# Performance work log

Measured on AMD Instinct MI355X. Metric: run time of the kernel, lower is better.

## Reference

```python
import jax, jax.numpy as jnp
import numpy as np

B, T, C, H = 4, 4096, 1024, 64


def setup_inputs() -> dict:
    key = jax.random.key(0)
    k1, k2, k3, k4 = jax.random.split(key, 4)
    x = jax.random.normal(k1, (B, T, C), dtype=jnp.float32)
    # nn.Linear(C, H, bias=False) weights, stored as [C, H] so y = x @ W
    Wq = jax.random.normal(k2, (C, H), dtype=jnp.float32) * (C ** -0.5)
    Wk = jax.random.normal(k3, (C, H), dtype=jnp.float32) * (C ** -0.5)
    Wv = jax.random.normal(k4, (C, H), dtype=jnp.float32) * (C ** -0.5)
    return {"x": x, "Wq": Wq, "Wk": Wk, "Wv": Wv}


def reference(x, Wq, Wk, Wv):
    # x: (B,T,C) -> q,k,v: (B,T,H)
    q = jnp.einsum('btc,ch->bth', x, Wq)
    k = jnp.einsum('btc,ch->bth', x, Wk)
    v = jnp.einsum('btc,ch->bth', x, Wv)
    scale = q.shape[-1] ** -0.5
    # (B,T,T) attention scores with causal mask
    scores = jnp.einsum('bqh,bkh->bqk', q, k) * scale
    t = x.shape[1]
    causal = jnp.tril(jnp.ones((t, t), dtype=bool))
    scores = jnp.where(causal, scores, -jnp.inf)
    attn = jax.nn.softmax(scores, axis=-1)
    return jnp.einsum('bqk,bkh->bqh', attn, v)
```

## Files before the change

kernel.cpp:

```cpp
#include <hip/hip_runtime.h>

#define BATCH 4
#define SEQ   4096
#define CDIM  1024
#define HDIM  64

typedef __attribute__((ext_vector_type(8))) short bf16x8;
typedef __attribute__((ext_vector_type(4))) float f32x4;

#define WT_OFF 0
#define Q_OFF  (3 * HDIM * CDIM)
#define KF_OFF (Q_OFF + BATCH * SEQ * HDIM)
#define VF_OFF (KF_OFF + BATCH * SEQ * HDIM)

static __device__ __forceinline__ short f2bf(float f) {
  union { float f; unsigned u; } a; a.f = f;
  unsigned r = a.u + 0x7fffu + ((a.u >> 16) & 1u);
  return (short)(r >> 16);
}

static __device__ __forceinline__ bf16x8 ld8(const short* p) {
  return *(const bf16x8*)p;
}

__global__ void wcvt_kernel(const float* __restrict__ wq, const float* __restrict__ wk,
                            const float* __restrict__ wv, short* __restrict__ wt2) {
  int idx = blockIdx.x * 256 + threadIdx.x;
  int m = idx >> 16;
  int f = idx & 65535;
  int k0g = f >> 11, hc = (f >> 9) & 3, lr = (f >> 5) & 15, lg = (f >> 3) & 3, j = f & 7;
  int c = k0g * 32 + lg * 8 + j, h = hc * 16 + lr;
  const float* w = (m == 0) ? wq : (m == 1) ? wk : wv;
  wt2[((k0g * 12 + m * 4 + hc) * 64 + lr * 4 + lg) * 8 + j] = f2bf(w[c * 64 + h]);
}

__global__ __launch_bounds__(512, 4) void proj_kernel(const float* __restrict__ x,
                                                      const short* __restrict__ wt2,
                                                      short* __restrict__ ws) {
  __shared__ short xs2[2][32 * 256];
  __shared__ short k_lds[8][16][24];
  __shared__ short v_lds[8][16][24];

  int tid = threadIdx.x;
  int widx = tid >> 6, lane = tid & 63;
  int lr = lane & 15, lg = lane >> 4;
  int row0 = blockIdx.x * 32;
  int rbh = widx >> 2;
  int hcw = widx & 3;

  int sr = tid >> 4, sci = tid & 15;
  const float* xsrc = x + (size_t)(row0 + sr) * CDIM + sci * 4;
  int sxor = (sr & 7) << 4;
  int sbase = sr * 512;

  int rowa = rbh * 16 + lr;
  int abase = rowa * 512;
  int axor = (rowa & 7) << 4;

  const short* bptr = wt2 + (hcw * 64 + lr * 4 + lg) * 8;

  f32x4 acc[3] = {};

#define PLOAD(RG, P) do {                                                    \
    _Pragma("unroll")                                                        \
    for (int q = 0; q < 4; ++q)                                              \
      RG[q] = *(const float4*)(xsrc + (P) * 256 + q * 64);                   \
  } while (0)

#define PSTORE(RG, BUF) do {                                                 \
    char* bc_ = (char*)&xs2[(BUF)][0];                                       \
    _Pragma("unroll")                                                        \
    for (int q = 0; q < 4; ++q) {                                            \
      uint2 u_;                                                              \
      u_.x = (unsigned)(unsigned short)f2bf(RG[q].x) |                       \
             ((unsigned)(unsigned short)f2bf(RG[q].y) << 16);                \
      u_.y = (unsigned)(unsigned short)f2bf(RG[q].z) |                       \
             ((unsigned)(unsigned short)f2bf(RG[q].w) << 16);                \
      *(uint2*)(bc_ + sbase + ((sci * 8 + q * 128) ^ sxor)) = u_;            \
    }                                                                        \
  } while (0)

#define PCOMPUTE(BUF, P) do {                                                \
    const char* bufc_ = (const char*)&xs2[(BUF)][0];                         \
    _Pragma("unroll")                                                        \
    for (int kk = 0; kk < 8; ++kk) {                                         \
      bf16x8 af_ = *(const bf16x8*)(bufc_ + abase + ((kk * 64 + lg * 16) ^ axor)); \
      const short* bk_ = bptr + ((P) * 8 + kk) * 6144;                       \
      _Pragma("unroll")                                                      \
      for (int m = 0; m < 3; ++m) {                                          \
        bf16x8 bf_ = ld8(bk_ + m * 2048);                                    \
        acc[m] = __builtin_amdgcn_mfma_f32_16x16x32_bf16(af_, bf_, acc[m], 0, 0, 0); \
      }                                                                      \
    }                                                                        \
  } while (0)

  {
    float4 rg[4];
    PLOAD(rg, 0);
    PSTORE(rg, 0);
  }
  __syncthreads();
#pragma unroll
  for (int p = 0; p < 4; ++p) {
    float4 rg[4];
    if (p < 3) PLOAD(rg, p + 1);
    PCOMPUTE(p & 1, p);
    if (p < 3) {
      PSTORE(rg, (p + 1) & 1);
      __syncthreads();
    }
  }

  short* qs  = ws + Q_OFF;
  short* kfr = ws + KF_OFF;
  short* vfr = ws + VF_OFF;
  int rbase = row0 + rbh * 16;
#pragma unroll
  for (int reg = 0; reg < 4; ++reg) {
    int t = rbase + lg * 4 + reg;
    qs[t * 64 + hcw * 16 + lr] = f2bf(acc[0][reg]);
    k_lds[widx][lg * 4 + reg][lr] = f2bf(acc[1][reg]);
    v_lds[widx][lr][lg * 4 + reg] = f2bf(acc[2][reg]);
  }
  int b = rbase >> 12;
  int tb = rbase & (SEQ - 1);
  int kb64 = tb >> 6, st = (tb >> 4) & 3;
  if (lane < 32) {
    int i0 = lane >> 1, f8 = (lane & 1) * 8;
    size_t kblk = ((((size_t)b * 64 + kb64) * 4 + st) * 2 + (hcw >> 1)) * 512;
    bf16x8 kv8 = *(const bf16x8*)(&k_lds[widx][i0][f8]);
    *(bf16x8*)(kfr + kblk + ((hcw & 1) * 2 + (f8 >> 3)) * 128 + i0 * 8) = kv8;
    size_t vblk = ((((size_t)b * 64 + kb64) * 2 + ((tb >> 5) & 1)) * 4 + hcw) * 512;
    bf16x8 vv8 = *(const bf16x8*)(&v_lds[widx][i0][f8]);
    *(bf16x8*)(vfr + vblk + (((tb & 16) + f8) >> 3) * 128 + i0 * 8) = vv8;
  }
}

__global__ __launch_bounds__(512, 4) void attn_kernel(const short* __restrict__ ws,
                                                      float* __restrict__ out) {
  __shared__ float p_o[8][4][4][64];
  __shared__ float p_l[8][4][64];
  __shared__ short plds[8][16][72];

  int widx = threadIdx.x >> 6, lane = threadIdx.x & 63;
  int lr = lane & 15, lg = lane >> 4;
  int g = blockIdx.x;

  const short* qs  = ws + Q_OFF;
  const short* kfr = ws + KF_OFF;
  const short* vfr = ws + VF_OFF;
  short* myp = &plds[widx][0][0];

  for (int tt = 0; tt < 2; ++tt) {
    int j = tt == 0 ? g : 1023 - g;
    int t16 = 255 - (j >> 2), b = j & 3;
    int qrow0 = b * SEQ + t16 * 16;
    int nkv = (t16 >> 2) + 1;

    bf16x8 qf0 = ld8(qs + (qrow0 + lr) * 64 + lg * 8);
    bf16x8 qf1 = ld8(qs + (qrow0 + lr) * 64 + 32 + lg * 8);
    const short* kb_b = kfr + (size_t)b * 64 * 4096 + lane * 8;
    const short* vb_b = vfr + (size_t)b * 64 * 4096 + lane * 8;

    f32x4 o[4] = {};
    float l_run[4] = {};

    if (tt) __syncthreads();

    bf16x8 kf[8];
    int kvb = widx;
    if (kvb < nkv) {
      const short* kb = kb_b + (size_t)kvb * 4096;
#pragma unroll
      for (int q8 = 0; q8 < 8; ++q8) kf[q8] = ld8(kb + q8 * 512);
    }

    for (; kvb < nkv; kvb += 8) {
      int kv0 = kvb * 64;

      f32x4 s[4] = {};
#pragma unroll
      for (int st = 0; st < 4; ++st) {
        s[st] = __builtin_amdgcn_mfma_f32_16x16x32_bf16(qf0, kf[st * 2],     s[st], 0, 0, 0);
        s[st] = __builtin_amdgcn_mfma_f32_16x16x32_bf16(qf1, kf[st * 2 + 1], s[st], 0, 0, 0);
      }

      bf16x8 vv[8];
      {
        const short* vb = vb_b + (size_t)kvb * 4096;
#pragma unroll
        for (int q8 = 0; q8 < 8; ++q8) vv[q8] = ld8(vb + q8 * 512);
      }
      int kvn = kvb + 8;
      if (kvn < nkv) {
        const short* kb = kb_b + (size_t)kvn * 4096;
#pragma unroll
        for (int q8 = 0; q8 < 8; ++q8) kf[q8] = ld8(kb + q8 * 512);
      }

      bool last = (kvb == nkv - 1);
#pragma unroll
      for (int reg = 0; reg < 4; ++reg) {
        int ig = t16 * 16 + lg * 4 + reg;
#pragma unroll
        for (int st = 0; st < 4; ++st) {
          float v = s[st][reg] * 0.125f;
          if (last && (kv0 + st * 16 + lr > ig)) v = -1e30f;
          float p = __expf(v);
          l_run[reg] += p;
          myp[(lg * 4 + reg) * 72 + st * 16 + lr] = f2bf(p);
        }
      }
      asm volatile("s_waitcnt lgkmcnt(0)" ::: "memory");
      bf16x8 pf0 = ld8(myp + lr * 72 + lg * 8);
      bf16x8 pf1 = ld8(myp + lr * 72 + 32 + lg * 8);

#pragma unroll
      for (int hc = 0; hc < 4; ++hc) {
        o[hc] = __builtin_amdgcn_mfma_f32_16x16x32_bf16(pf0, vv[hc],     o[hc], 0, 0, 0);
        o[hc] = __builtin_amdgcn_mfma_f32_16x16x32_bf16(pf1, vv[4 + hc], o[hc], 0, 0, 0);
      }
    }

#pragma unroll
    for (int reg = 0; reg < 4; ++reg) {
      float l = l_run[reg];
      l += __shfl_xor(l, 1);
      l += __shfl_xor(l, 2);
      l += __shfl_xor(l, 4);
      l += __shfl_xor(l, 8);
      l_run[reg] = l;
    }

#pragma unroll
    for (int hc = 0; hc < 4; ++hc)
#pragma unroll
      for (int reg = 0; reg < 4; ++reg)
        p_o[widx][hc][reg][lane] = o[hc][reg];
#pragma unroll
    for (int reg = 0; reg < 4; ++reg)
      p_l[widx][reg][lane] = l_run[reg];
    __syncthreads();

    if (widx < 4) {
      int reg = widx;
      float lsum = 0.f;
#pragma unroll
      for (int w = 0; w < 8; ++w) lsum += p_l[w][reg][lane];
      float inv = 1.0f / lsum;
#pragma unroll
      for (int hc = 0; hc < 4; ++hc) {
        float sv = 0.f;
#pragma unroll
        for (int w = 0; w < 8; ++w) sv += p_o[w][hc][reg][lane];
        out[(qrow0 + lg * 4 + reg) * 64 + hc * 16 + lr] = sv * inv;
      }
    }
  }
}

extern "C" void kernel_launch(void* const* d_in, const int* in_sizes, int n_in,
                              void* d_out, int out_size, void* d_ws, size_t ws_size,
                              hipStream_t stream) {
  const float* x  = (const float*)d_in[0];
  const float* wq = (const float*)d_in[1];
  const float* wk = (const float*)d_in[2];
  const float* wv = (const float*)d_in[3];
  short* ws = (short*)d_ws;
  float* out = (float*)d_out;

  wcvt_kernel<<<dim3(768), dim3(256), 0, stream>>>(wq, wk, wv, ws + WT_OFF);
  proj_kernel<<<dim3(512), dim3(512), 0, stream>>>(x, ws + WT_OFF, ws);
  attn_kernel<<<dim3(512), dim3(512), 0, stream>>>(ws, out);
}
```

Before: 67.30 us.

## Split QKV projection across 12 waves, one output tile each, with contiguous x loads

The projection kernel moves from 8 waves to 12 waves per block. Each wave now owns one (matrix, head-chunk) pair and computes both 16-row tiles, so the weight fragment is loaded once per wave and reused across two MFMAs. Before, each wave loaded three weight fragments per A fragment. The x staging loads change from strided float4s to four contiguous float4s per thread, with only the first 512 threads staging. The trade-off is more threads per block, idle staging threads, and higher register and launch-bounds pressure.

```diff
diff --git a/kernel.cpp b/kernel.cpp
--- a/kernel.cpp
+++ b/kernel.cpp
@@ -34,37 +34,36 @@
   wt2[((k0g * 12 + m * 4 + hc) * 64 + lr * 4 + lg) * 8 + j] = f2bf(w[c * 64 + h]);
 }
 
-__global__ __launch_bounds__(512, 4) void proj_kernel(const float* __restrict__ x,
+__global__ __launch_bounds__(768, 6) void proj_kernel(const float* __restrict__ x,
                                                       const short* __restrict__ wt2,
                                                       short* __restrict__ ws) {
   __shared__ short xs2[2][32 * 256];
-  __shared__ short k_lds[8][16][24];
-  __shared__ short v_lds[8][16][24];
+  __shared__ short k_lds[4][2][16][16];
+  __shared__ short v_lds[4][2][16][16];
 
   int tid = threadIdx.x;
   int widx = tid >> 6, lane = tid & 63;
   int lr = lane & 15, lg = lane >> 4;
   int row0 = blockIdx.x * 32;
-  int rbh = widx >> 2;
-  int hcw = widx & 3;
+  int p = widx;
+  int m = p >> 2, hcw = p & 3;
 
   int sr = tid >> 4, sci = tid & 15;
-  const float* xsrc = x + (size_t)(row0 + sr) * CDIM + sci * 4;
+  const float* xsrc = x + (size_t)(row0 + sr) * CDIM + sci * 16;
+  int sbase = sr * 512;
   int sxor = (sr & 7) << 4;
-  int sbase = sr * 512;
-
-  int rowa = rbh * 16 + lr;
-  int abase = rowa * 512;
-  int axor = (rowa & 7) << 4;
-
-  const short* bptr = wt2 + (hcw * 64 + lr * 4 + lg) * 8;
-
-  f32x4 acc[3] = {};
+
+  int abase0 = lr * 512, abase1 = (16 + lr) * 512;
+  int axor = (lr & 7) << 4;
+
+  const short* bptr = wt2 + p * 512 + (lr * 4 + lg) * 8;
+
+  f32x4 acc[2] = {};
 
 #define PLOAD(RG, P) do {                                                    \
     _Pragma("unroll")                                                        \
     for (int q = 0; q < 4; ++q)                                              \
-      RG[q] = *(const float4*)(xsrc + (P) * 256 + q * 64);                   \
+      RG[q] = *(const float4*)(xsrc + (P) * 256 + q * 4);                    \
   } while (0)
 
 #define PSTORE(RG, BUF) do {                                                 \
@@ -76,7 +75,7 @@
              ((unsigned)(unsigned short)f2bf(RG[q].y) << 16);                \
       u_.y = (unsigned)(unsigned short)f2bf(RG[q].z) |                       \
              ((unsigned)(unsigned short)f2bf(RG[q].w) << 16);                \
-      *(uint2*)(bc_ + sbase + ((sci * 8 + q * 128) ^ sxor)) = u_;            \
+      *(uint2*)(bc_ + sbase + ((sci * 32 + q * 8) ^ sxor)) = u_;             \
     }                                                                        \
   } while (0)
 
@@ -84,29 +83,28 @@
     const char* bufc_ = (const char*)&xs2[(BUF)][0];                         \
     _Pragma("unroll")                                                        \
     for (int kk = 0; kk < 8; ++kk) {                                         \
-      bf16x8 af_ = *(const bf16x8*)(bufc_ + abase + ((kk * 64 + lg * 16) ^ axor)); \
-      const short* bk_ = bptr + ((P) * 8 + kk) * 6144;                       \
-      _Pragma("unroll")                                                      \
-      for (int m = 0; m < 3; ++m) {                                          \
-        bf16x8 bf_ = ld8(bk_ + m * 2048);                                    \
-        acc[m] = __builtin_amdgcn_mfma_f32_16x16x32_bf16(af_, bf_, acc[m], 0, 0, 0); \
-      }                                                                      \
+      int co_ = (kk * 64 + lg * 16) ^ axor;                                  \
+      bf16x8 af0_ = *(const bf16x8*)(bufc_ + abase0 + co_);                  \
+      bf16x8 af1_ = *(const bf16x8*)(bufc_ + abase1 + co_);                  \
+      bf16x8 bf_  = ld8(bptr + ((P) * 8 + kk) * 6144);                       \
+      acc[0] = __builtin_amdgcn_mfma_f32_16x16x32_bf16(af0_, bf_, acc[0], 0, 0, 0); \
+      acc[1] = __builtin_amdgcn_mfma_f32_16x16x32_bf16(af1_, bf_, acc[1], 0, 0, 0); \
     }                                                                        \
   } while (0)
 
-  {
+  if (tid < 512) {
     float4 rg[4];
     PLOAD(rg, 0);
     PSTORE(rg, 0);
   }
   __syncthreads();
 #pragma unroll
-  for (int p = 0; p < 4; ++p) {
+  for (int ph = 0; ph < 4; ++ph) {
     float4 rg[4];
-    if (p < 3) PLOAD(rg, p + 1);
-    PCOMPUTE(p & 1, p);
-    if (p < 3) {
-      PSTORE(rg, (p + 1) & 1);
+    if (ph < 3 && tid < 512) PLOAD(rg, ph + 1);
+    PCOMPUTE(ph & 1, ph);
+    if (ph < 3) {
+      if (tid < 512) PSTORE(rg, (ph + 1) & 1);
       __syncthreads();
     }
   }
@@ -114,25 +112,51 @@
   short* qs  = ws + Q_OFF;
   short* kfr = ws + KF_OFF;
   short* vfr = ws + VF_OFF;
-  int rbase = row0 + rbh * 16;
-#pragma unroll
-  for (int reg = 0; reg < 4; ++reg) {
-    int t = rbase + lg * 4 + reg;
-    qs[t * 64 + hcw * 16 + lr] = f2bf(acc[0][reg]);
-    k_lds[widx][lg * 4 + reg][lr] = f2bf(acc[1][reg]);
-    v_lds[widx][lr][lg * 4 + reg] = f2bf(acc[2][reg]);
-  }
-  int b = rbase >> 12;
-  int tb = rbase & (SEQ - 1);
-  int kb64 = tb >> 6, st = (tb >> 4) & 3;
-  if (lane < 32) {
-    int i0 = lane >> 1, f8 = (lane & 1) * 8;
-    size_t kblk = ((((size_t)b * 64 + kb64) * 4 + st) * 2 + (hcw >> 1)) * 512;
-    bf16x8 kv8 = *(const bf16x8*)(&k_lds[widx][i0][f8]);
-    *(bf16x8*)(kfr + kblk + ((hcw & 1) * 2 + (f8 >> 3)) * 128 + i0 * 8) = kv8;
-    size_t vblk = ((((size_t)b * 64 + kb64) * 2 + ((tb >> 5) & 1)) * 4 + hcw) * 512;
-    bf16x8 vv8 = *(const bf16x8*)(&v_lds[widx][i0][f8]);
-    *(bf16x8*)(vfr + vblk + (((tb & 16) + f8) >> 3) * 128 + i0 * 8) = vv8;
+
+  if (m == 0) {
+#pragma unroll
+    for (int rt = 0; rt < 2; ++rt) {
+      int rbase = row0 + rt * 16;
+#pragma unroll
+      for (int reg = 0; reg < 4; ++reg)
+        qs[(rbase + lg * 4 + reg) * 64 + hcw * 16 + lr] = f2bf(acc[rt][reg]);
+    }
+  } else if (m == 1) {
+#pragma unroll
+    for (int rt = 0; rt < 2; ++rt)
+#pragma unroll
+      for (int reg = 0; reg < 4; ++reg)
+        k_lds[hcw][rt][lg * 4 + reg][lr] = f2bf(acc[rt][reg]);
+    if (lane < 32) {
+      int i0 = lane >> 1, f8 = (lane & 1) * 8;
+#pragma unroll
+      for (int rt = 0; rt < 2; ++rt) {
+        int rbase = row0 + rt * 16;
+        int b = rbase >> 12, tb = rbase & (SEQ - 1);
+        int kb64 = tb >> 6, st = (tb >> 4) & 3;
+        size_t kblk = ((((size_t)b * 64 + kb64) * 4 + st) * 2 + (hcw >> 1)) * 512;
+        bf16x8 kv8 = *(const bf16x8*)(&k_lds[hcw][rt][i0][f8]);
+        *(bf16x8*)(kfr + kblk + ((hcw & 1) * 2 + (f8 >> 3)) * 128 + i0 * 8) = kv8;
+      }
+    }
+  } else {
+#pragma unroll
+    for (int rt = 0; rt < 2; ++rt)
+#pragma unroll
+      for (int reg = 0; reg < 4; ++reg)
+        v_lds[hcw][rt][lr][lg * 4 + reg] = f2bf(acc[rt][reg]);
+    if (lane < 32) {
+      int i0 = lane >> 1, f8 = (lane & 1) * 8;
+#pragma unroll
+      for (int rt = 0; rt < 2; ++rt) {
+        int rbase = row0 + rt * 16;
+        int b = rbase >> 12, tb = rbase & (SEQ - 1);
+        int kb64 = tb >> 6;
+        size_t vblk = ((((size_t)b * 64 + kb64) * 2 + ((tb >> 5) & 1)) * 4 + hcw) * 512;
+        bf16x8 vv8 = *(const bf16x8*)(&v_lds[hcw][rt][i0][f8]);
+        *(bf16x8*)(vfr + vblk + (((tb & 16) + f8) >> 3) * 128 + i0 * 8) = vv8;
+      }
+    }
   }
 }
 
@@ -270,6 +294,6 @@
   float* out = (float*)d_out;
 
   wcvt_kernel<<<dim3(768), dim3(256), 0, stream>>>(wq, wk, wv, ws + WT_OFF);
-  proj_kernel<<<dim3(512), dim3(512), 0, stream>>>(x, ws + WT_OFF, ws);
+  proj_kernel<<<dim3(512), dim3(768), 0, stream>>>(x, ws + WT_OFF, ws);
   attn_kernel<<<dim3(512), dim3(512), 0, stream>>>(ws, out);
 }
```

Result: faster. 60.04 us (-10.8%).
